# Kernel tuning notes

Hardware: AMD Instinct MI355X
Metric: run time of the kernel (lower is better)

## Reference

```python
import jax, jax.numpy as jnp
import numpy as np

EPS = 1e-8  # torch F.cosine_similarity eps
TEMP = 2.0  # hardcoded in module regardless of init arg


def _normalize(x):
    # row-normalize with torch-style eps clamp on the norm
    norm = jnp.sqrt(jnp.sum(x * x, axis=-1, keepdims=True))
    return x / jnp.maximum(norm, EPS)


def setup_inputs() -> dict:
    key = jax.random.key(0)
    k1, k2, k3 = jax.random.split(key, 3)
    n, m, d = 8192, 8192, 256
    return {
        "pos_key": jax.random.normal(k1, (n, d), dtype=jnp.float32),
        "pos_value": jax.random.normal(k2, (n, d), dtype=jnp.float32),
        "neg_value": jax.random.normal(k3, (m, d), dtype=jnp.float32),
    }


def reference(pos_key, pos_value, neg_value):
    pk = _normalize(pos_key)    # [n, d]
    pv = _normalize(pos_value)  # [n, d]
    nv = _normalize(neg_value)  # [m, d]

    pos_sim = jnp.sum(pk * pv, axis=-1)          # [n]
    neg_sim = jnp.einsum("nd,md->nm", pk, nv)    # [n, m] cosine sims

    pos_loss = -jnp.mean(pos_sim / TEMP)
    # log-sum-exp over m (stable), matching log(sum(exp(.)))
    neg_loss = jnp.mean(jax.scipy.special.logsumexp(neg_sim / TEMP, axis=-1))
    return pos_loss + neg_loss
```

## Files before the change

kernel.cpp:

```cpp
#include <hip/hip_runtime.h>

typedef __attribute__((ext_vector_type(4))) float f32x4;
typedef __attribute__((ext_vector_type(4))) int   i32x4;
typedef __attribute__((ext_vector_type(8))) int   i32x8;

#define DIM 256
#define D4  64

#define GLD_LDS16(g, l) __builtin_amdgcn_global_load_lds(                      \
    (const __attribute__((address_space(1))) void*)(g),                        \
    (__attribute__((address_space(3))) void*)(l), 16, 0, 0)

__global__ __launch_bounds__(256) void normalize_kernel(
    const float4* __restrict__ pk, const float4* __restrict__ pv,
    const float4* __restrict__ nv, unsigned int* __restrict__ pkn,
    unsigned int* __restrict__ nvn, float* __restrict__ posPart, int N) {
  int row  = blockIdx.x * 4 + (threadIdx.x >> 6);
  int lane = threadIdx.x & 63;
  if (row < N) {
    float4 x = pk[row * D4 + lane];
    float4 y = pv[row * D4 + lane];
    float skk = x.x*x.x + x.y*x.y + x.z*x.z + x.w*x.w;
    float svv = y.x*y.x + y.y*y.y + y.z*y.z + y.w*y.w;
    float skv = x.x*y.x + x.y*y.y + x.z*y.z + x.w*y.w;
#pragma unroll
    for (int m = 32; m >= 1; m >>= 1) {
      skk += __shfl_xor(skk, m, 64);
      svv += __shfl_xor(svv, m, 64);
      skv += __shfl_xor(skv, m, 64);
    }
    float nk  = fmaxf(sqrtf(skk), 1e-8f);
    float nvv = fmaxf(sqrtf(svv), 1e-8f);
    if (lane == 0) posPart[row] = skv / (nk * nvv);
    float rk = 1.0f / nk;
    int w = __builtin_amdgcn_cvt_pk_fp8_f32(x.x * rk, x.y * rk, 0, false);
    w = __builtin_amdgcn_cvt_pk_fp8_f32(x.z * rk, x.w * rk, w, true);
    pkn[(size_t)row * 64 + lane] = (unsigned int)w;
  } else {
    int r2 = row - N;
    float4 x = nv[r2 * D4 + lane];
    float s = x.x*x.x + x.y*x.y + x.z*x.z + x.w*x.w;
#pragma unroll
    for (int m = 32; m >= 1; m >>= 1) s += __shfl_xor(s, m, 64);
    float rn = 1.0f / fmaxf(sqrtf(s), 1e-8f);
    int w = __builtin_amdgcn_cvt_pk_fp8_f32(x.x * rn, x.y * rn, 0, false);
    w = __builtin_amdgcn_cvt_pk_fp8_f32(x.z * rn, x.w * rn, w, true);
    nvn[(size_t)r2 * 64 + lane] = (unsigned int)w;
  }
}

__global__ __launch_bounds__(512, 2) void gemm_lse_kernel(
    const unsigned char* __restrict__ gA, const unsigned char* __restrict__ gB,
    float* __restrict__ partial, int N) {
  __shared__ unsigned char As[65536];
  __shared__ unsigned char Bs[2][32768];

  const int tid  = threadIdx.x;
  const int lane = tid & 63;
  const int wv   = tid >> 6;
  const int wm   = wv >> 1;
  const int wn   = wv & 1;
  const int l15  = lane & 15, q = lane >> 4;
  const int cg    = blockIdx.x;
  const int panel = blockIdx.y;
  const int row0  = panel * 256;
  const int colBase = cg * 1024;
  const float kLog2eHalf = 0.72134752044448170f;
  const int kUnitScale = 0x7F7F7F7F;

  auto stageB = [&](int t) {
    const unsigned char* src = gB + (size_t)(colBase + t * 128) * 256;
    unsigned char* dst = &Bs[t & 1][0];
#pragma unroll
    for (int kb = 0; kb < 2; kb++)
#pragma unroll
      for (int i = 0; i < 2; i++) {
        int c  = i * 512 + tid;
        int r  = c >> 3;
        int sc = ((c & 7) ^ (r & 7)) << 4;
        GLD_LDS16(src + (size_t)r * 256 + kb * 128 + sc,
                  dst + kb * 16384 + c * 16);
      }
  };

#pragma unroll
  for (int kb = 0; kb < 2; kb++)
#pragma unroll
    for (int i = 0; i < 4; i++) {
      int c  = i * 512 + tid;
      int r  = c >> 3;
      int sc = ((c & 7) ^ (r & 7)) << 4;
      GLD_LDS16(gA + (size_t)(row0 + r) * 256 + kb * 128 + sc,
                As + kb * 32768 + c * 16);
    }
  stageB(0);
  stageB(1);
  asm volatile("s_waitcnt vmcnt(4)\n\ts_barrier" ::: "memory");

#pragma unroll 2
  for (int t = 0; t < 8; t++) {
    if (t) {
      asm volatile("s_waitcnt vmcnt(1)\n\ts_barrier" ::: "memory");
      if (t < 7) stageB(t + 1);
    }
    const unsigned char* bufB = &Bs[t & 1][0];

    f32x4 acc[4][4];
#pragma unroll
    for (int mi = 0; mi < 4; mi++)
#pragma unroll
      for (int ni = 0; ni < 4; ni++) acc[mi][ni] = (f32x4){0.f, 0.f, 0.f, 0.f};

#pragma unroll
    for (int kb = 0; kb < 2; kb++) {
      i32x8 bf[4];
#pragma unroll
      for (int ni = 0; ni < 4; ni++) {
        int r  = wn * 64 + ni * 16 + l15;
        int c0 = (q * 2)     ^ (r & 7);
        int c1 = (q * 2 + 1) ^ (r & 7);
        i32x4 lo = *(const i32x4*)(bufB + kb * 16384 + r * 128 + c0 * 16);
        i32x4 hi = *(const i32x4*)(bufB + kb * 16384 + r * 128 + c1 * 16);
        bf[ni] = (i32x8){lo.x, lo.y, lo.z, lo.w, hi.x, hi.y, hi.z, hi.w};
      }
#pragma unroll
      for (int mi = 0; mi < 4; mi++) {
        int r  = wm * 64 + mi * 16 + l15;
        int c0 = (q * 2)     ^ (r & 7);
        int c1 = (q * 2 + 1) ^ (r & 7);
        i32x4 lo = *(const i32x4*)(As + kb * 32768 + r * 128 + c0 * 16);
        i32x4 hi = *(const i32x4*)(As + kb * 32768 + r * 128 + c1 * 16);
        i32x8 af = (i32x8){lo.x, lo.y, lo.z, lo.w, hi.x, hi.y, hi.z, hi.w};
        __builtin_amdgcn_s_setprio(1);
#pragma unroll
        for (int ni = 0; ni < 4; ni++)
          acc[mi][ni] = __builtin_amdgcn_mfma_scale_f32_16x16x128_f8f6f4(
              bf[ni], af, acc[mi][ni],
              0, 0, 0, kUnitScale, 0, kUnitScale);
        __builtin_amdgcn_s_setprio(0);
      }
    }

    float s0, s1, s2, s3;
#pragma unroll
    for (int mi = 0; mi < 4; mi++) {
      float v = 0.f;
#pragma unroll
      for (int ni = 0; ni < 4; ni++)
#pragma unroll
        for (int rr = 0; rr < 4; rr++)
          v += __builtin_amdgcn_exp2f(acc[mi][ni][rr] * kLog2eHalf);
      v += __shfl_xor(v, 16, 64);
      v += __shfl_xor(v, 32, 64);
      if (mi == 0) s0 = v; else if (mi == 1) s1 = v;
      else if (mi == 2) s2 = v; else s3 = v;
    }
    float o = q == 0 ? s0 : q == 1 ? s1 : q == 2 ? s2 : s3;
    int slab = cg * 16 + t * 2 + wn;
    partial[(size_t)slab * N + row0 + wm * 64 + q * 16 + l15] = o;
  }
}

__global__ __launch_bounds__(256) void finalize_kernel(
    const float* __restrict__ partial, const float* __restrict__ posPart,
    float* __restrict__ out, int N, int slabsPerGroup, float invN) {
  __shared__ float red[4][64];
  int t  = threadIdx.x;
  int rl = t & 63, g = t >> 6;
  int row = blockIdx.x * 64 + rl;
  const float* p = partial + (size_t)(g * slabsPerGroup) * N + row;
  float s = 0.f;
#pragma unroll 8
  for (int j = 0; j < slabsPerGroup; j++) s += p[(size_t)j * N];
  red[g][rl] = s;
  __syncthreads();
  if (t < 64) {
    float tot = red[0][rl] + red[1][rl] + red[2][rl] + red[3][rl];
    float v = __builtin_amdgcn_logf(tot) * 0.69314718055994531f
              - 0.5f * posPart[row];
#pragma unroll
    for (int m = 32; m >= 1; m >>= 1) v += __shfl_xor(v, m, 64);
    if (rl == 0) atomicAdd(out, v * invN);
  }
}

extern "C" void kernel_launch(void* const* d_in, const int* in_sizes, int n_in,
                              void* d_out, int out_size, void* d_ws, size_t ws_size,
                              hipStream_t stream) {
  const float* pk = (const float*)d_in[0];
  const float* pv = (const float*)d_in[1];
  const float* nv = (const float*)d_in[2];
  int N = in_sizes[0] / DIM;
  int M = in_sizes[2] / DIM;
  float* out = (float*)d_out;

  unsigned char* pkn = (unsigned char*)d_ws;
  unsigned char* nvn = pkn + (size_t)N * DIM;
  float* partial = (float*)(nvn + (size_t)M * DIM);
  float* posPart = partial + (size_t)(M / 64) * N;

  hipMemsetAsync(out, 0, sizeof(float), stream);

  normalize_kernel<<<(N + M) / 4, 256, 0, stream>>>(
      (const float4*)pk, (const float4*)pv, (const float4*)nv,
      (unsigned int*)pkn, (unsigned int*)nvn, posPart, N);

  gemm_lse_kernel<<<dim3(M / 1024, N / 256), 512, 0, stream>>>(
      pkn, nvn, partial, N);

  finalize_kernel<<<N / 64, 256, 0, stream>>>(
      partial, posPart, out, N, (M / 64) / 4, 1.0f / (float)N);
}
```

Before: 101.0 us.

## Keep A fragments in registers and deepen B LDS pipeline to four buffers

The A panel is no longer staged through shared memory. Each wave loads its fp8 A fragments straight from global memory into registers once, which removes the A LDS reads from the inner loop. The LDS this frees is used to quadruple-buffer B tiles with three tiles in flight. Hand-tuned vmcnt waits per fully unrolled iteration track the outstanding loads, trading higher VGPR pressure and fragile wait counts for less LDS traffic and deeper prefetch.

```diff
diff --git a/kernel.cpp b/kernel.cpp
--- a/kernel.cpp
+++ b/kernel.cpp
@@ -10,6 +10,8 @@
 #define GLD_LDS16(g, l) __builtin_amdgcn_global_load_lds(                      \
     (const __attribute__((address_space(1))) void*)(g),                        \
     (__attribute__((address_space(3))) void*)(l), 16, 0, 0)
+
+#define TILE_WAIT(N) asm volatile("s_waitcnt vmcnt(" #N ")\n\ts_barrier" ::: "memory")
 
 __global__ __launch_bounds__(256) void normalize_kernel(
     const float4* __restrict__ pk, const float4* __restrict__ pv,
@@ -52,8 +54,7 @@
 __global__ __launch_bounds__(512, 2) void gemm_lse_kernel(
     const unsigned char* __restrict__ gA, const unsigned char* __restrict__ gB,
     float* __restrict__ partial, int N) {
-  __shared__ unsigned char As[65536];
-  __shared__ unsigned char Bs[2][32768];
+  __shared__ unsigned char Bs[4][32768];
 
   const int tid  = threadIdx.x;
   const int lane = tid & 63;
@@ -70,7 +71,7 @@
 
   auto stageB = [&](int t) {
     const unsigned char* src = gB + (size_t)(colBase + t * 128) * 256;
-    unsigned char* dst = &Bs[t & 1][0];
+    unsigned char* dst = &Bs[t & 3][0];
 #pragma unroll
     for (int kb = 0; kb < 2; kb++)
 #pragma unroll
@@ -83,28 +84,37 @@
       }
   };
 
+  const unsigned char* aB = gA + (size_t)(row0 + wm * 64 + l15) * 256 + q * 32;
+  i32x8 af[2][4];
 #pragma unroll
   for (int kb = 0; kb < 2; kb++)
 #pragma unroll
-    for (int i = 0; i < 4; i++) {
-      int c  = i * 512 + tid;
-      int r  = c >> 3;
-      int sc = ((c & 7) ^ (r & 7)) << 4;
-      GLD_LDS16(gA + (size_t)(row0 + r) * 256 + kb * 128 + sc,
-                As + kb * 32768 + c * 16);
-    }
+    for (int mi = 0; mi < 4; mi++)
+      af[kb][mi] = *(const i32x8*)(aB + mi * 16 * 256 + kb * 128);
+  __builtin_amdgcn_sched_barrier(0);
+
   stageB(0);
   stageB(1);
-  asm volatile("s_waitcnt vmcnt(4)\n\ts_barrier" ::: "memory");
-
-#pragma unroll 2
+  stageB(2);
+  __builtin_amdgcn_sched_barrier(0);
+
+#pragma unroll
   for (int t = 0; t < 8; t++) {
-    if (t) {
-      asm volatile("s_waitcnt vmcnt(1)\n\ts_barrier" ::: "memory");
-      if (t < 7) stageB(t + 1);
-    }
-    const unsigned char* bufB = &Bs[t & 1][0];
-
+    if      (t == 0) TILE_WAIT(7);
+    else if (t == 1) TILE_WAIT(8);
+    else if (t == 2) TILE_WAIT(9);
+    else if (t == 3) TILE_WAIT(10);
+    else if (t == 4) TILE_WAIT(10);
+    else if (t == 5) TILE_WAIT(10);
+    else if (t == 6) TILE_WAIT(6);
+    else             TILE_WAIT(2);
+
+    if (t < 5) {
+      stageB(t + 3);
+      __builtin_amdgcn_sched_barrier(0);
+    }
+
+    const unsigned char* bufB = &Bs[t & 3][0];
     f32x4 acc[4][4];
 #pragma unroll
     for (int mi = 0; mi < 4; mi++)
@@ -125,17 +135,11 @@
       }
 #pragma unroll
       for (int mi = 0; mi < 4; mi++) {
-        int r  = wm * 64 + mi * 16 + l15;
-        int c0 = (q * 2)     ^ (r & 7);
-        int c1 = (q * 2 + 1) ^ (r & 7);
-        i32x4 lo = *(const i32x4*)(As + kb * 32768 + r * 128 + c0 * 16);
-        i32x4 hi = *(const i32x4*)(As + kb * 32768 + r * 128 + c1 * 16);
-        i32x8 af = (i32x8){lo.x, lo.y, lo.z, lo.w, hi.x, hi.y, hi.z, hi.w};
         __builtin_amdgcn_s_setprio(1);
 #pragma unroll
         for (int ni = 0; ni < 4; ni++)
           acc[mi][ni] = __builtin_amdgcn_mfma_scale_f32_16x16x128_f8f6f4(
-              bf[ni], af, acc[mi][ni],
+              bf[ni], af[kb][mi], acc[mi][ni],
               0, 0, 0, kUnitScale, 0, kUnitScale);
         __builtin_amdgcn_s_setprio(0);
       }
@@ -158,6 +162,7 @@
     float o = q == 0 ? s0 : q == 1 ? s1 : q == 2 ? s2 : s3;
     int slab = cg * 16 + t * 2 + wn;
     partial[(size_t)slab * N + row0 + wm * 64 + q * 16 + l15] = o;
+    __builtin_amdgcn_sched_barrier(0);
   }
 }
 
```

Result: no change. 101.0 us (-0.0%).
